# Kernel tuning notes

Hardware: AMD Instinct MI355X
Metric: run time of the kernel (lower is better)

Reference implementation:

```python
import jax, jax.numpy as jnp
import numpy as np


def _conv3x3(x, w, b):
    # NCHW conv, stride 1, pad 1
    y = jax.lax.conv_general_dilated(x, w, (1, 1), ((1, 1), (1, 1)),
                                     dimension_numbers=('NCHW', 'OIHW', 'NCHW'))
    return y + b[None, :, None, None]


def _deform_conv3x3(x, offset, w):
    # Deformable conv v1: 3x3, stride 1, pad 1, 1 deformable group, no bias.
    # offset: [B, 18, H, W] laid out as (dy_k, dx_k) for k = 0..8 (row-major taps).
    B, C, H, W = x.shape
    K = 9
    off = offset.reshape(B, K, 2, H, W)
    ky, kx = jnp.meshgrid(jnp.arange(3), jnp.arange(3), indexing='ij')
    ky = (ky.reshape(K) - 1).astype(x.dtype)  # kernel tap y-offset, pad=1
    kx = (kx.reshape(K) - 1).astype(x.dtype)
    hh = jnp.arange(H, dtype=x.dtype)
    ww = jnp.arange(W, dtype=x.dtype)
    # sampling locations [B, K, H, W]
    sy = hh[None, None, :, None] + ky[None, :, None, None] + off[:, :, 0]
    sx = ww[None, None, None, :] + kx[None, :, None, None] + off[:, :, 1]
    y0 = jnp.floor(sy)
    x0 = jnp.floor(sx)
    ly = sy - y0  # fractional parts
    lx = sx - x0
    x_flat = x.reshape(B, C, H * W)

    def gather(yi, xi, wgt):
        # zero-padding semantics: corners outside the image contribute 0
        valid = (yi >= 0) & (yi < H) & (xi >= 0) & (xi < W)
        idx = (jnp.clip(yi, 0, H - 1).astype(jnp.int32) * W
               + jnp.clip(xi, 0, W - 1).astype(jnp.int32)).reshape(B, 1, K * H * W)
        v = jnp.take_along_axis(x_flat, idx, axis=2).reshape(B, C, K, H, W)
        return v * (wgt * valid.astype(x.dtype))[:, None]

    sampled = (gather(y0,     x0,     (1 - ly) * (1 - lx))
             + gather(y0,     x0 + 1, (1 - ly) * lx)
             + gather(y0 + 1, x0,     ly * (1 - lx))
             + gather(y0 + 1, x0 + 1, ly * lx))  # [B, C, K, H, W]
    return jnp.einsum('bckhw,ock->bohw', sampled, w.reshape(w.shape[0], C, K))


def setup_inputs() -> dict:
    key = jax.random.key(0)
    ks = jax.random.split(key, 8)
    C, O = 256, 256
    return {
        'kernel': jax.random.normal(ks[0], (16, C, 16, 16), jnp.float32),
        'search': jax.random.normal(ks[1], (16, C, 32, 32), jnp.float32),
        'Toffset_w': jax.random.normal(ks[2], (18, C, 3, 3), jnp.float32) * 0.02,
        'Toffset_b': jnp.zeros((18,), jnp.float32),
        'Tdeform_w': jax.random.normal(ks[3], (O, C, 3, 3), jnp.float32) * 0.02,
        'Soffset_w': jax.random.normal(ks[4], (18, C, 3, 3), jnp.float32) * 0.02,
        'Soffset_b': jnp.zeros((18,), jnp.float32),
        'Sdeform_w': jax.random.normal(ks[5], (O, C, 3, 3), jnp.float32) * 0.02,
    }


def reference(kernel, search, Toffset_w, Toffset_b, Tdeform_w,
              Soffset_w, Soffset_b, Sdeform_w):
    kernel_offset = _conv3x3(kernel, Toffset_w, Toffset_b)
    kernel_out = _deform_conv3x3(kernel, kernel_offset, Tdeform_w)
    search_offset = _conv3x3(search, Soffset_w, Soffset_b)
    search_out = _deform_conv3x3(search, search_offset, Sdeform_w)
    return (kernel_out, search_out, kernel_offset, search_offset)
```

## Files before the change

### kernel.cpp

```cpp
#include <hip/hip_runtime.h>

#define CIN   256
#define OC    256
#define K_TOT 2304
#define CCH   32
#define NCHK  8
#define KCH   288
#define SSTR  296
#define DM    64

#define N_DW  (OC * K_TOT)
#define N_OW  (32 * K_TOT)
#define N_CVT (2 * N_DW + 2 * N_OW)
#define CVT_BLOCKS (N_CVT / 4 / 512)
#define XT_K_ELEMS ((size_t)16 * 256 * 256)
#define XT_S_ELEMS ((size_t)16 * 1024 * 256)

typedef short  bf16x8 __attribute__((ext_vector_type(8)));
typedef float  f32x4  __attribute__((ext_vector_type(4)));
typedef unsigned short ushort_t;

__device__ __forceinline__ ushort_t f2bf(float f) {
    unsigned u = __builtin_bit_cast(unsigned, f);
    u += 0x7fffu + ((u >> 16) & 1u);
    return (ushort_t)(u >> 16);
}
__device__ __forceinline__ float bf2f(short s) {
    return __builtin_bit_cast(float, ((unsigned)(unsigned short)s) << 16);
}

__global__ __launch_bounds__(512) void prep_k(
    const float* __restrict__ tdw, const float* __restrict__ sdw,
    const float* __restrict__ tow, const float* __restrict__ sow,
    const float* __restrict__ kin, const float* __restrict__ sin_,
    ushort_t* __restrict__ wk_d, ushort_t* __restrict__ ws_d,
    ushort_t* __restrict__ wk_o, ushort_t* __restrict__ ws_o,
    ushort_t* __restrict__ xt_k, ushort_t* __restrict__ xt_s)
{
    __shared__ ushort_t tile[64][264];

    if (blockIdx.x == 0 && threadIdx.x < 64) {
        ushort4 z = {0, 0, 0, 0};
        *(ushort4*)&xt_s[XT_S_ELEMS + (size_t)threadIdx.x * 4] = z;
    }

    if (blockIdx.x < CVT_BLOCKS) {
        const int i = (blockIdx.x * 512 + threadIdx.x) * 4;
        const float* src; ushort_t* dst; int j; bool offw = false;
        if (i < N_DW)                    { src = tdw; dst = wk_d; j = i; }
        else if (i < 2 * N_DW)           { src = sdw; dst = ws_d; j = i - N_DW; }
        else if (i < 2 * N_DW + N_OW)    { src = tow; dst = wk_o; j = i - 2 * N_DW; offw = true; }
        else                             { src = sow; dst = ws_o; j = i - 2 * N_DW - N_OW; offw = true; }
        const int oc = j / K_TOT;
        const int k  = j - oc * K_TOT;
        const int cc = k / KCH;
        const int r  = k - cc * KCH;
        const int tap = r >> 5;
        const int cl  = r & 31;
        ushort4 o4 = {0, 0, 0, 0};
        if (!offw || oc < 18) {
            const float* sp = &src[((size_t)oc * CIN + cc * 32 + cl) * 9 + tap];
            o4.x = f2bf(sp[0]); o4.y = f2bf(sp[9]); o4.z = f2bf(sp[18]); o4.w = f2bf(sp[27]);
        }
        *(ushort4*)&dst[j] = o4;
        return;
    }

    const int bx2 = blockIdx.x - CVT_BLOCKS;
    int H, W, b, px0; const float* x; ushort_t* xt;
    if (bx2 < 64) {
        H = 16; W = 16; x = kin; xt = xt_k;
        b = bx2 >> 2; px0 = (bx2 & 3) * 64;
    } else {
        int t2 = bx2 - 64;
        H = 32; W = 32; x = sin_; xt = xt_s;
        b = t2 >> 4; px0 = (t2 & 15) * 64;
    }
    const int HW = H * W;
    const int t = threadIdx.x, lane = t & 63, wv = t >> 6;
    const float* xb = x + (size_t)b * CIN * HW;

    for (int it = 0; it < 8; ++it) {
        const int ch = wv * 32 + it * 4 + (lane >> 4);
        const int pq = (lane & 15) * 4;
        float4 v = *(const float4*)&xb[(size_t)ch * HW + px0 + pq];
        tile[pq + 0][ch] = f2bf(v.x);
        tile[pq + 1][ch] = f2bf(v.y);
        tile[pq + 2][ch] = f2bf(v.z);
        tile[pq + 3][ch] = f2bf(v.w);
    }
    __syncthreads();
    for (int it = 0; it < 4; ++it) {
        const int px = it * 16 + wv * 2 + (lane >> 5);
        const int cg = (lane & 31) * 8;
        bf16x8 v = *(const bf16x8*)&tile[px][cg];
        *(bf16x8*)&xt[((size_t)b * HW + px0 + px) * 256 + cg] = v;
    }
}

__global__ __launch_bounds__(512, 2) void conv_gemm_k(
    const ushort_t* __restrict__ xt_k, const ushort_t* __restrict__ kwgt,
    const float* __restrict__ kbias, float* __restrict__ kout,
    const ushort_t* __restrict__ xt_s, const ushort_t* __restrict__ swgt,
    const float* __restrict__ sbias, float* __restrict__ sout)
{
    __shared__ float sred[7][64][36];

    int H, W, sh, b, px0; int zrel;
    const ushort_t* xt; const ushort_t* wgt; const float* bias; float* out;
    if (blockIdx.x < 64) {
        const int xcd = blockIdx.x & 7, i = blockIdx.x >> 3;
        H = 16; W = 16; sh = 4; xt = xt_k; wgt = kwgt; bias = kbias; out = kout;
        b = xcd + 8 * (i & 1); px0 = (i >> 1) * 64;
        zrel = (int)(XT_K_ELEMS + XT_S_ELEMS - (size_t)b * 256 * 256);
    } else {
        const int t2 = blockIdx.x - 64;
        const int xcd = t2 & 7, i = t2 >> 3;
        H = 32; W = 32; sh = 5; xt = xt_s; wgt = swgt; bias = sbias; out = sout;
        b = xcd + 8 * (i & 1); px0 = (i >> 1) * 64;
        zrel = (int)(XT_S_ELEMS - (size_t)b * 1024 * 256);
    }
    const int HW = H * W;
    const int t = threadIdx.x, lane = t & 63, kh = t >> 6;
    const int l15 = lane & 15;
    const int cg8 = (lane >> 4) * 8;
    const ushort_t* xtb = xt + (size_t)b * HW * 256;

    int h[4], wc[4];
#pragma unroll
    for (int mt = 0; mt < 4; ++mt) {
        const int px = px0 + mt * 16 + l15;
        h[mt]  = px >> sh;
        wc[mt] = px & (W - 1);
    }
    const ushort_t* wrow0 = wgt + (size_t)(l15)      * K_TOT + cg8;
    const ushort_t* wrow1 = wgt + (size_t)(16 + l15) * K_TOT + cg8;
    const int cb = kh * 32 + cg8;
    const size_t kg0 = (size_t)kh * KCH;

    f32x4 acc[4][2] = {};
#pragma unroll
    for (int ks = 0; ks < 9; ++ks) {
        const bf16x8 b0 = *(const bf16x8*)&wrow0[kg0 + (size_t)ks * 32];
        const bf16x8 b1 = *(const bf16x8*)&wrow1[kg0 + (size_t)ks * 32];
        const int dy = ks / 3 - 1, dx = ks % 3 - 1;
        bf16x8 a[4];
#pragma unroll
        for (int mt = 0; mt < 4; ++mt) {
            const int y  = h[mt] + dy;
            const int xx = wc[mt] + dx;
            const bool ok = ((unsigned)y < (unsigned)H) && ((unsigned)xx < (unsigned)W);
            const int off = ok ? (((y << sh) + xx) * 256 + cb) : (zrel + cb);
            a[mt] = *(const bf16x8*)&xtb[off];
        }
#pragma unroll
        for (int mt = 0; mt < 4; ++mt) {
            acc[mt][0] = __builtin_amdgcn_mfma_f32_16x16x32_bf16(a[mt], b0, acc[mt][0], 0, 0, 0);
            acc[mt][1] = __builtin_amdgcn_mfma_f32_16x16x32_bf16(a[mt], b1, acc[mt][1], 0, 0, 0);
        }
    }

    if (kh > 0) {
#pragma unroll
        for (int mt = 0; mt < 4; ++mt)
#pragma unroll
            for (int nt = 0; nt < 2; ++nt)
                *(float4*)&sred[kh - 1][lane][(mt * 2 + nt) * 4] = *(float4*)&acc[mt][nt];
    }
    __syncthreads();
    if (kh == 0) {
        const int prow = (lane >> 4) * 4;
#pragma unroll
        for (int nt = 0; nt < 2; ++nt) {
            const int oc = nt * 16 + l15;
            if (oc < 18) {
                const float bs = bias[oc];
#pragma unroll
                for (int mt = 0; mt < 4; ++mt) {
                    float4 r = *(float4*)&acc[mt][nt];
#pragma unroll
                    for (int q = 0; q < 7; ++q) {
                        const float4 o = *(const float4*)&sred[q][lane][(mt * 2 + nt) * 4];
                        r.x += o.x; r.y += o.y; r.z += o.z; r.w += o.w;
                    }
                    r.x += bs; r.y += bs; r.z += bs; r.w += bs;
                    *(float4*)(out + ((size_t)b * 18 + oc) * HW + px0 + mt * 16 + prow) = r;
                }
            }
        }
    }
}

__device__ __forceinline__ void dcn_load4(
    bf16x8* c, const ushort_t* __restrict__ xtb, int4 id, int cb)
{
    c[0] = *(const bf16x8*)&xtb[(size_t)id.x * 256 + cb];
    c[1] = *(const bf16x8*)&xtb[(size_t)id.y * 256 + cb];
    c[2] = *(const bf16x8*)&xtb[(size_t)id.z * 256 + cb];
    c[3] = *(const bf16x8*)&xtb[(size_t)id.w * 256 + cb];
}
__device__ __forceinline__ void dcn_proc2(
    ushort_t* swb, int so, const bf16x8* c, float4 wt)
{
    bf16x8 r;
#pragma unroll
    for (int j = 0; j < 8; ++j) {
        const float v = wt.x * bf2f(c[0][j]) + wt.y * bf2f(c[1][j])
                      + wt.z * bf2f(c[2][j]) + wt.w * bf2f(c[3][j]);
        r[j] = (short)f2bf(v);
    }
    *(bf16x8*)&swb[so] = r;
}

__global__ __launch_bounds__(512, 4) void deform_gemm_k(
    const ushort_t* __restrict__ xt_k, const float* __restrict__ koffs,
    const ushort_t* __restrict__ kwgt, float* __restrict__ kout,
    const ushort_t* __restrict__ xt_s, const float* __restrict__ soffs,
    const ushort_t* __restrict__ swgt_, float* __restrict__ sout)
{
    __shared__ __align__(16) ushort_t smp[DM][SSTR];
    __shared__ __align__(16) int      sidx[DM][9][4];
    __shared__ __align__(16) float    swt [DM][9][4];

    int H, W, b, px0;
    const ushort_t* xt; const float* offs; const ushort_t* wgt; float* out;
    if (blockIdx.x < 64) {
        const int xcd = blockIdx.x & 7, i = blockIdx.x >> 3;
        H = 16; W = 16; xt = xt_k; offs = koffs; wgt = kwgt; out = kout;
        b = xcd + 8 * (i & 1); px0 = (i >> 1) * 64;
    } else {
        const int t2 = blockIdx.x - 64;
        const int xcd = t2 & 7, i = t2 >> 3;
        H = 32; W = 32; xt = xt_s; offs = soffs; wgt = swgt_; out = sout;
        b = xcd + 8 * (i & 1); px0 = (i >> 1) * 64;
    }
    const int HW = H * W;
    const int t = threadIdx.x, lane = t & 63, wv = t >> 6;

#pragma unroll
    for (int u = 0; u < 2; ++u) {
        const int s = t + u * 512;
        if (s < DM * 9) {
            const int p = s / 9, k = s - 9 * p;
            const int pix = px0 + p;
            const int h  = pix / W;
            const int wc = pix - h * W;
            const float* ob = offs + (size_t)b * 18 * HW;
            const float dy = ob[(2 * k    ) * HW + pix];
            const float dx = ob[(2 * k + 1) * HW + pix];
            const float sy = (float)(h  + k / 3 - 1) + dy;
            const float sx = (float)(wc + k % 3 - 1) + dx;
            const float y0f = floorf(sy), x0f = floorf(sx);
            const float ly = sy - y0f, lx = sx - x0f;
            const int y0 = (int)y0f, x0 = (int)x0f;
#pragma unroll
            for (int j = 0; j < 4; ++j) {
                const int yy = y0 + (j >> 1);
                const int xx = x0 + (j & 1);
                const bool ok = ((unsigned)yy < (unsigned)H) && ((unsigned)xx < (unsigned)W);
                sidx[p][k][j] = min(max(yy, 0), H - 1) * W + min(max(xx, 0), W - 1);
                const float wj = ((j >> 1) ? ly : 1.f - ly) * ((j & 1) ? lx : 1.f - lx);
                swt[p][k][j] = ok ? wj : 0.f;
            }
        }
    }
    __syncthreads();

    const ushort_t* xtb = xt + (size_t)b * HW * 256;
    const int l15 = lane & 15;
    const int cg8 = (lane >> 4) * 8;
    const int ocb = wv * 32;
    const bool live4 = (t < 256);

    const int g0  = t >> 2;
    const int cgE = (t & 3) * 8;
    int uso[5];
#pragma unroll
    for (int q = 0; q < 5; ++q) {
        const int g  = g0 + q * 128;
        const int px = g / 9, tap = g - 9 * px;
        uso[q] = px * SSTR + tap * 32 + (t & 3) * 8;
    }

    const ushort_t* wrow0 = wgt + (size_t)(ocb      + l15) * K_TOT + cg8;
    const ushort_t* wrow1 = wgt + (size_t)(ocb + 16 + l15) * K_TOT + cg8;
    ushort_t* smpb = &smp[0][0];
    const int4*   sidxF = (const int4*)  &sidx[0][0][0];
    const float4* swtF  = (const float4*)&swt [0][0][0];

    f32x4 acc[4][2] = {};

    for (int cc = 0; cc < NCHK; ++cc) {
        const int cb = cc * 32 + cgE;
        const size_t kg0 = (size_t)cc * KCH;

        bf16x8 cA[4], cB[4];
        float4 wA, wB;
        bf16x8 bq[2][2];
        { const int4 id = sidxF[g0];       wA = swtF[g0];       dcn_load4(cA, xtb, id, cb); }
        { const int4 id = sidxF[g0 + 128]; wB = swtF[g0 + 128]; dcn_load4(cB, xtb, id, cb); }
        bq[0][0] = *(const bf16x8*)&wrow0[kg0];
        bq[0][1] = *(const bf16x8*)&wrow1[kg0];

        dcn_proc2(smpb, uso[0], cA, wA);
        { const int4 id = sidxF[g0 + 256]; wA = swtF[g0 + 256]; dcn_load4(cA, xtb, id, cb); }
        dcn_proc2(smpb, uso[1], cB, wB);
        { const int4 id = sidxF[g0 + 384]; wB = swtF[g0 + 384]; dcn_load4(cB, xtb, id, cb); }
        dcn_proc2(smpb, uso[2], cA, wA);
        if (live4) { const int4 id = sidxF[g0 + 512]; wA = swtF[g0 + 512]; dcn_load4(cA, xtb, id, cb); }
        dcn_proc2(smpb, uso[3], cB, wB);
        if (live4) dcn_proc2(smpb, uso[4], cA, wA);

        asm volatile("s_waitcnt lgkmcnt(0)" ::: "memory");
        __builtin_amdgcn_sched_barrier(0);
        __builtin_amdgcn_s_barrier();
        __builtin_amdgcn_sched_barrier(0);

        __builtin_amdgcn_s_setprio(1);
#pragma unroll
        for (int ks = 0; ks < 9; ++ks) {
            if (ks < 8) {
                bq[(ks + 1) & 1][0] = *(const bf16x8*)&wrow0[kg0 + (size_t)(ks + 1) * 32];
                bq[(ks + 1) & 1][1] = *(const bf16x8*)&wrow1[kg0 + (size_t)(ks + 1) * 32];
            }
            bf16x8 a[4];
#pragma unroll
            for (int mt = 0; mt < 4; ++mt)
                a[mt] = *(const bf16x8*)&smp[mt * 16 + l15][ks * 32 + cg8];
#pragma unroll
            for (int mt = 0; mt < 4; ++mt) {
                acc[mt][0] = __builtin_amdgcn_mfma_f32_16x16x32_bf16(a[mt], bq[ks & 1][0], acc[mt][0], 0, 0, 0);
                acc[mt][1] = __builtin_amdgcn_mfma_f32_16x16x32_bf16(a[mt], bq[ks & 1][1], acc[mt][1], 0, 0, 0);
            }
        }
        __builtin_amdgcn_s_setprio(0);

        if (cc < NCHK - 1) {
            __builtin_amdgcn_sched_barrier(0);
            __builtin_amdgcn_s_barrier();
            __builtin_amdgcn_sched_barrier(0);
        }
    }

    const int prow = (lane >> 4) * 4;
#pragma unroll
    for (int mt = 0; mt < 4; ++mt) {
#pragma unroll
        for (int nt = 0; nt < 2; ++nt) {
            const int oc = ocb + nt * 16 + l15;
            float* op = out + ((size_t)b * OC + oc) * HW + px0 + mt * 16 + prow;
            *(float4*)op = *(float4*)&acc[mt][nt];
        }
    }
}

extern "C" void kernel_launch(void* const* d_in, const int* in_sizes, int n_in,
                              void* d_out, int out_size, void* d_ws, size_t ws_size,
                              hipStream_t stream) {
    const float* kin = (const float*)d_in[0];
    const float* sin_ = (const float*)d_in[1];
    const float* tow = (const float*)d_in[2];
    const float* tob = (const float*)d_in[3];
    const float* tdw = (const float*)d_in[4];
    const float* sow = (const float*)d_in[5];
    const float* sob = (const float*)d_in[6];
    const float* sdw = (const float*)d_in[7];

    float* out = (float*)d_out;
    float* out_k  = out;
    float* out_s  = out_k + (size_t)16 * 256 * 16 * 16;
    float* out_ko = out_s + (size_t)16 * 256 * 32 * 32;
    float* out_so = out_ko + (size_t)16 * 18 * 16 * 16;

    ushort_t* wk_d = (ushort_t*)d_ws;
    ushort_t* ws_d = wk_d + N_DW;
    ushort_t* wk_o = ws_d + N_DW;
    ushort_t* ws_o = wk_o + N_OW;
    ushort_t* xt_k = ws_o + N_OW;
    ushort_t* xt_s = xt_k + XT_K_ELEMS;

    prep_k<<<dim3(CVT_BLOCKS + 320), 512, 0, stream>>>(
        tdw, sdw, tow, sow, kin, sin_,
        wk_d, ws_d, wk_o, ws_o, xt_k, xt_s);

    conv_gemm_k<<<dim3(320), 512, 0, stream>>>(
        xt_k, wk_o, tob, out_ko, xt_s, ws_o, sob, out_so);

    deform_gemm_k<<<dim3(320), 512, 0, stream>>>(
        xt_k, out_ko, wk_d, out_k, xt_s, out_so, ws_d, out_s);
}
```

Baseline: 205.6 us.

## Fuse offset conv into deformable GEMM kernel via shared-memory offsets

Merges the offset-prediction conv kernel into the deformable conv kernel. Each block computes the offsets for its own 64 pixels, stores them to global output and to shared memory, then builds the bilinear sampling tables from shared memory instead of re-reading global offsets. This removes one kernel launch and the global round trip of the offsets. In exchange the fused kernel uses more shared memory through a union buffer and has higher register pressure under launch_bounds(512,4), which may reduce occupancy.

```diff
diff --git a/kernel.cpp b/kernel.cpp
--- a/kernel.cpp
+++ b/kernel.cpp
@@ -98,99 +98,6 @@
     }
 }
 
-__global__ __launch_bounds__(512, 2) void conv_gemm_k(
-    const ushort_t* __restrict__ xt_k, const ushort_t* __restrict__ kwgt,
-    const float* __restrict__ kbias, float* __restrict__ kout,
-    const ushort_t* __restrict__ xt_s, const ushort_t* __restrict__ swgt,
-    const float* __restrict__ sbias, float* __restrict__ sout)
-{
-    __shared__ float sred[7][64][36];
-
-    int H, W, sh, b, px0; int zrel;
-    const ushort_t* xt; const ushort_t* wgt; const float* bias; float* out;
-    if (blockIdx.x < 64) {
-        const int xcd = blockIdx.x & 7, i = blockIdx.x >> 3;
-        H = 16; W = 16; sh = 4; xt = xt_k; wgt = kwgt; bias = kbias; out = kout;
-        b = xcd + 8 * (i & 1); px0 = (i >> 1) * 64;
-        zrel = (int)(XT_K_ELEMS + XT_S_ELEMS - (size_t)b * 256 * 256);
-    } else {
-        const int t2 = blockIdx.x - 64;
-        const int xcd = t2 & 7, i = t2 >> 3;
-        H = 32; W = 32; sh = 5; xt = xt_s; wgt = swgt; bias = sbias; out = sout;
-        b = xcd + 8 * (i & 1); px0 = (i >> 1) * 64;
-        zrel = (int)(XT_S_ELEMS - (size_t)b * 1024 * 256);
-    }
-    const int HW = H * W;
-    const int t = threadIdx.x, lane = t & 63, kh = t >> 6;
-    const int l15 = lane & 15;
-    const int cg8 = (lane >> 4) * 8;
-    const ushort_t* xtb = xt + (size_t)b * HW * 256;
-
-    int h[4], wc[4];
-#pragma unroll
-    for (int mt = 0; mt < 4; ++mt) {
-        const int px = px0 + mt * 16 + l15;
-        h[mt]  = px >> sh;
-        wc[mt] = px & (W - 1);
-    }
-    const ushort_t* wrow0 = wgt + (size_t)(l15)      * K_TOT + cg8;
-    const ushort_t* wrow1 = wgt + (size_t)(16 + l15) * K_TOT + cg8;
-    const int cb = kh * 32 + cg8;
-    const size_t kg0 = (size_t)kh * KCH;
-
-    f32x4 acc[4][2] = {};
-#pragma unroll
-    for (int ks = 0; ks < 9; ++ks) {
-        const bf16x8 b0 = *(const bf16x8*)&wrow0[kg0 + (size_t)ks * 32];
-        const bf16x8 b1 = *(const bf16x8*)&wrow1[kg0 + (size_t)ks * 32];
-        const int dy = ks / 3 - 1, dx = ks % 3 - 1;
-        bf16x8 a[4];
-#pragma unroll
-        for (int mt = 0; mt < 4; ++mt) {
-            const int y  = h[mt] + dy;
-            const int xx = wc[mt] + dx;
-            const bool ok = ((unsigned)y < (unsigned)H) && ((unsigned)xx < (unsigned)W);
-            const int off = ok ? (((y << sh) + xx) * 256 + cb) : (zrel + cb);
-            a[mt] = *(const bf16x8*)&xtb[off];
-        }
-#pragma unroll
-        for (int mt = 0; mt < 4; ++mt) {
-            acc[mt][0] = __builtin_amdgcn_mfma_f32_16x16x32_bf16(a[mt], b0, acc[mt][0], 0, 0, 0);
-            acc[mt][1] = __builtin_amdgcn_mfma_f32_16x16x32_bf16(a[mt], b1, acc[mt][1], 0, 0, 0);
-        }
-    }
-
-    if (kh > 0) {
-#pragma unroll
-        for (int mt = 0; mt < 4; ++mt)
-#pragma unroll
-            for (int nt = 0; nt < 2; ++nt)
-                *(float4*)&sred[kh - 1][lane][(mt * 2 + nt) * 4] = *(float4*)&acc[mt][nt];
-    }
-    __syncthreads();
-    if (kh == 0) {
-        const int prow = (lane >> 4) * 4;
-#pragma unroll
-        for (int nt = 0; nt < 2; ++nt) {
-            const int oc = nt * 16 + l15;
-            if (oc < 18) {
-                const float bs = bias[oc];
-#pragma unroll
-                for (int mt = 0; mt < 4; ++mt) {
-                    float4 r = *(float4*)&acc[mt][nt];
-#pragma unroll
-                    for (int q = 0; q < 7; ++q) {
-                        const float4 o = *(const float4*)&sred[q][lane][(mt * 2 + nt) * 4];
-                        r.x += o.x; r.y += o.y; r.z += o.z; r.w += o.w;
-                    }
-                    r.x += bs; r.y += bs; r.z += bs; r.w += bs;
-                    *(float4*)(out + ((size_t)b * 18 + oc) * HW + px0 + mt * 16 + prow) = r;
-                }
-            }
-        }
-    }
-}
-
 __device__ __forceinline__ void dcn_load4(
     bf16x8* c, const ushort_t* __restrict__ xtb, int4 id, int cb)
 {
@@ -213,29 +120,113 @@
 }
 
 __global__ __launch_bounds__(512, 4) void deform_gemm_k(
-    const ushort_t* __restrict__ xt_k, const float* __restrict__ koffs,
-    const ushort_t* __restrict__ kwgt, float* __restrict__ kout,
-    const ushort_t* __restrict__ xt_s, const float* __restrict__ soffs,
-    const ushort_t* __restrict__ swgt_, float* __restrict__ sout)
+    const ushort_t* __restrict__ xt_k,
+    const ushort_t* __restrict__ kwo, const float* __restrict__ kbias,
+    float* __restrict__ koff, const ushort_t* __restrict__ kwd,
+    float* __restrict__ kout,
+    const ushort_t* __restrict__ xt_s,
+    const ushort_t* __restrict__ swo, const float* __restrict__ sbias,
+    float* __restrict__ soff, const ushort_t* __restrict__ swd,
+    float* __restrict__ sout)
 {
-    __shared__ __align__(16) ushort_t smp[DM][SSTR];
-    __shared__ __align__(16) int      sidx[DM][9][4];
-    __shared__ __align__(16) float    swt [DM][9][4];
-
-    int H, W, b, px0;
-    const ushort_t* xt; const float* offs; const ushort_t* wgt; float* out;
+    __shared__ __align__(16) char  uni[64512];
+    __shared__ __align__(16) float offsL[18][64];
+
+    float    (*sred)[64][36] = (float(*)[64][36])uni;
+    ushort_t (*smp)[SSTR]    = (ushort_t(*)[SSTR])uni;
+    int      (*sidx)[9][4]   = (int(*)[9][4])(uni + 37888);
+    float    (*swt)[9][4]    = (float(*)[9][4])(uni + 47104);
+
+    int H, W, sh, b, px0; int zrel;
+    const ushort_t *xt, *wgo, *wgd; const float* bias; float *ooff, *out;
     if (blockIdx.x < 64) {
         const int xcd = blockIdx.x & 7, i = blockIdx.x >> 3;
-        H = 16; W = 16; xt = xt_k; offs = koffs; wgt = kwgt; out = kout;
+        H = 16; W = 16; sh = 4; xt = xt_k; wgo = kwo; bias = kbias;
+        ooff = koff; wgd = kwd; out = kout;
         b = xcd + 8 * (i & 1); px0 = (i >> 1) * 64;
+        zrel = (int)(XT_K_ELEMS + XT_S_ELEMS - (size_t)b * 256 * 256);
     } else {
         const int t2 = blockIdx.x - 64;
         const int xcd = t2 & 7, i = t2 >> 3;
-        H = 32; W = 32; xt = xt_s; offs = soffs; wgt = swgt_; out = sout;
+        H = 32; W = 32; sh = 5; xt = xt_s; wgo = swo; bias = sbias;
+        ooff = soff; wgd = swd; out = sout;
         b = xcd + 8 * (i & 1); px0 = (i >> 1) * 64;
+        zrel = (int)(XT_S_ELEMS - (size_t)b * 1024 * 256);
     }
     const int HW = H * W;
     const int t = threadIdx.x, lane = t & 63, wv = t >> 6;
+    const int l15 = lane & 15;
+    const int cg8 = (lane >> 4) * 8;
+    const ushort_t* xtb = xt + (size_t)b * HW * 256;
+
+    {
+        const int kh = wv;
+        int h[4], wc[4];
+#pragma unroll
+        for (int mt = 0; mt < 4; ++mt) {
+            const int px = px0 + mt * 16 + l15;
+            h[mt]  = px >> sh;
+            wc[mt] = px & (W - 1);
+        }
+        const ushort_t* wrow0 = wgo + (size_t)(l15)      * K_TOT + cg8;
+        const ushort_t* wrow1 = wgo + (size_t)(16 + l15) * K_TOT + cg8;
+        const int cb = kh * 32 + cg8;
+        const size_t kg0 = (size_t)kh * KCH;
+
+        f32x4 acc[4][2] = {};
+#pragma unroll
+        for (int ks = 0; ks < 9; ++ks) {
+            const bf16x8 b0 = *(const bf16x8*)&wrow0[kg0 + (size_t)ks * 32];
+            const bf16x8 b1 = *(const bf16x8*)&wrow1[kg0 + (size_t)ks * 32];
+            const int dy = ks / 3 - 1, dx = ks % 3 - 1;
+            bf16x8 a[4];
+#pragma unroll
+            for (int mt = 0; mt < 4; ++mt) {
+                const int y  = h[mt] + dy;
+                const int xx = wc[mt] + dx;
+                const bool ok = ((unsigned)y < (unsigned)H) && ((unsigned)xx < (unsigned)W);
+                const int off = ok ? (((y << sh) + xx) * 256 + cb) : (zrel + cb);
+                a[mt] = *(const bf16x8*)&xtb[off];
+            }
+#pragma unroll
+            for (int mt = 0; mt < 4; ++mt) {
+                acc[mt][0] = __builtin_amdgcn_mfma_f32_16x16x32_bf16(a[mt], b0, acc[mt][0], 0, 0, 0);
+                acc[mt][1] = __builtin_amdgcn_mfma_f32_16x16x32_bf16(a[mt], b1, acc[mt][1], 0, 0, 0);
+            }
+        }
+
+        if (kh > 0) {
+#pragma unroll
+            for (int mt = 0; mt < 4; ++mt)
+#pragma unroll
+                for (int nt = 0; nt < 2; ++nt)
+                    *(float4*)&sred[kh - 1][lane][(mt * 2 + nt) * 4] = *(float4*)&acc[mt][nt];
+        }
+        __syncthreads();
+        if (kh == 0) {
+            const int prow = (lane >> 4) * 4;
+#pragma unroll
+            for (int nt = 0; nt < 2; ++nt) {
+                const int oc = nt * 16 + l15;
+                if (oc < 18) {
+                    const float bs = bias[oc];
+#pragma unroll
+                    for (int mt = 0; mt < 4; ++mt) {
+                        float4 r = *(float4*)&acc[mt][nt];
+#pragma unroll
+                        for (int q = 0; q < 7; ++q) {
+                            const float4 o = *(const float4*)&sred[q][lane][(mt * 2 + nt) * 4];
+                            r.x += o.x; r.y += o.y; r.z += o.z; r.w += o.w;
+                        }
+                        r.x += bs; r.y += bs; r.z += bs; r.w += bs;
+                        *(float4*)(ooff + ((size_t)b * 18 + oc) * HW + px0 + mt * 16 + prow) = r;
+                        *(float4*)&offsL[oc][mt * 16 + prow] = r;
+                    }
+                }
+            }
+        }
+        __syncthreads();
+    }
 
 #pragma unroll
     for (int u = 0; u < 2; ++u) {
@@ -243,13 +234,12 @@
         if (s < DM * 9) {
             const int p = s / 9, k = s - 9 * p;
             const int pix = px0 + p;
-            const int h  = pix / W;
-            const int wc = pix - h * W;
-            const float* ob = offs + (size_t)b * 18 * HW;
-            const float dy = ob[(2 * k    ) * HW + pix];
-            const float dx = ob[(2 * k + 1) * HW + pix];
-            const float sy = (float)(h  + k / 3 - 1) + dy;
-            const float sx = (float)(wc + k % 3 - 1) + dx;
+            const int hh = pix >> sh;
+            const int ww = pix & (W - 1);
+            const float dy = offsL[2 * k    ][p];
+            const float dx = offsL[2 * k + 1][p];
+            const float sy = (float)(hh + k / 3 - 1) + dy;
+            const float sx = (float)(ww + k % 3 - 1) + dx;
             const float y0f = floorf(sy), x0f = floorf(sx);
             const float ly = sy - y0f, lx = sx - x0f;
             const int y0 = (int)y0f, x0 = (int)x0f;
@@ -266,9 +256,6 @@
     }
     __syncthreads();
 
-    const ushort_t* xtb = xt + (size_t)b * HW * 256;
-    const int l15 = lane & 15;
-    const int cg8 = (lane >> 4) * 8;
     const int ocb = wv * 32;
     const bool live4 = (t < 256);
 
@@ -282,8 +269,8 @@
         uso[q] = px * SSTR + tap * 32 + (t & 3) * 8;
     }
 
-    const ushort_t* wrow0 = wgt + (size_t)(ocb      + l15) * K_TOT + cg8;
-    const ushort_t* wrow1 = wgt + (size_t)(ocb + 16 + l15) * K_TOT + cg8;
+    const ushort_t* wrow0 = wgd + (size_t)(ocb      + l15) * K_TOT + cg8;
+    const ushort_t* wrow1 = wgd + (size_t)(ocb + 16 + l15) * K_TOT + cg8;
     ushort_t* smpb = &smp[0][0];
     const int4*   sidxF = (const int4*)  &sidx[0][0][0];
     const float4* swtF  = (const float4*)&swt [0][0][0];
@@ -383,9 +370,7 @@
         tdw, sdw, tow, sow, kin, sin_,
         wk_d, ws_d, wk_o, ws_o, xt_k, xt_s);
 
-    conv_gemm_k<<<dim3(320), 512, 0, stream>>>(
-        xt_k, wk_o, tob, out_ko, xt_s, ws_o, sob, out_so);
-
     deform_gemm_k<<<dim3(320), 512, 0, stream>>>(
-        xt_k, out_ko, wk_d, out_k, xt_s, out_so, ws_d, out_s);
-}
+        xt_k, wk_o, tob, out_ko, wk_d, out_k,
+        xt_s, ws_o, sob, out_so, ws_d, out_s);
+}
```

New measurement: 201.1 us. -2.2%, faster.
